# Performance work log

Measured on AMD Instinct MI355X. Metric: run time of the kernel, lower is better.

## Reference

```python
import jax, jax.numpy as jnp
import numpy as np

H = 1024   # hidden_dim
L = 2      # n_layers
V = 512    # dict_size['target']
B = 256    # batch
S = 512    # encoder seq len
IN = 64    # maxlen['input'][0] = encoder input feature dim
T = 64     # maxlen['target'] = decoder steps


def setup_inputs() -> dict:
    key = jax.random.key(0)
    ks = jax.random.split(key, 16)
    def p(k, shape):
        return jax.random.normal(k, shape, jnp.float32) * 0.05
    emb = p(ks[0], (V, H)).at[0].set(0.0)  # padding_idx=0 row is zero
    return dict(
        x=jax.random.normal(ks[1], (B, S, IN), jnp.float32),
        emb=emb,
        enc_Wih0=p(ks[2], (3 * H, IN)), enc_Whh0=p(ks[3], (3 * H, H)),
        enc_bih0=p(ks[4], (3 * H,)),   enc_bhh0=p(ks[5], (3 * H,)),
        enc_Wih1=p(ks[6], (3 * H, H)), enc_Whh1=p(ks[7], (3 * H, H)),
        enc_bih1=p(ks[8], (3 * H,)),   enc_bhh1=p(ks[9], (3 * H,)),
        dec_Wih=p(ks[10], (L, 3 * H, H)), dec_Whh=p(ks[11], (L, 3 * H, H)),
        dec_bih=p(ks[12], (L, 3 * H)),    dec_bhh=p(ks[13], (L, 3 * H)),
        fc_W=p(ks[14], (V, H)), fc_b=p(ks[15], (V,)),
    )


def gru_cell(x, h, Wih, Whh, bih, bhh):
    # torch GRU cell: r,z,n gate ordering
    gx = x @ Wih.T + bih            # (B, 3H)
    gh = h @ Whh.T + bhh            # (B, 3H)
    rx, zx, nx = jnp.split(gx, 3, axis=-1)
    rh, zh, nh = jnp.split(gh, 3, axis=-1)
    r = jax.nn.sigmoid(rx + rh)
    z = jax.nn.sigmoid(zx + zh)
    n = jnp.tanh(nx + r * nh)
    return (1.0 - z) * n + z * h


def reference(x, emb, enc_Wih0, enc_Whh0, enc_bih0, enc_bhh0,
              enc_Wih1, enc_Whh1, enc_bih1, enc_bhh1,
              dec_Wih, dec_Whh, dec_bih, dec_bhh, fc_W, fc_b):
    b = x.shape[0]
    # ---------- encoder: 2-layer unidirectional GRU ----------
    seq = jnp.swapaxes(x, 0, 1)  # (S, B, IN) time-major for scan
    enc_params = [(enc_Wih0, enc_Whh0, enc_bih0, enc_bhh0),
                  (enc_Wih1, enc_Whh1, enc_bih1, enc_bhh1)]
    finals = []
    for (Wih, Whh, bih, bhh) in enc_params:
        h0 = jnp.zeros((b, H), seq.dtype)
        def step(h, xt, Wih=Wih, Whh=Whh, bih=bih, bhh=bhh):
            hn = gru_cell(xt, h, Wih, Whh, bih, bhh)
            return hn, hn
        hT, seq = jax.lax.scan(step, h0, seq)
        finals.append(hT)
    hidden = jnp.stack(finals)  # (L, B, H)

    tok0 = jnp.zeros((b,), jnp.int32)  # start token 0 (== <pad>)

    def dec_step(carry, _):
        hcur, tok = carry
        inp = emb[tok]                       # (B, H) embedding lookup
        new_h = []
        for l in range(L):
            hn = gru_cell(inp, hcur[l], dec_Wih[l], dec_Whh[l],
                          dec_bih[l], dec_bhh[l])
            new_h.append(hn)
            inp = hn
        logits = inp @ fc_W.T + fc_b         # (B, V)
        tok = jnp.argmax(logits, axis=-1).astype(jnp.int32)
        return (jnp.stack(new_h), tok), logits

    (h_fin, _), logits_seq = jax.lax.scan(dec_step, (hidden, tok0), None, length=T)
    out = jnp.swapaxes(logits_seq, 0, 1)     # (B, T, V)
    return out, h_fin
```

## Files before the change

kernel.cpp:

```cpp
#include <hip/hip_runtime.h>
#include <math.h>

namespace {

constexpr int BSZ = 256;
constexpr int SEQ = 512;
constexpr int KIN = 64;
constexpr int HID = 1024;
constexpr int GD  = 3072;
constexpr int VOC = 512;
constexpr int TT  = 64;

typedef _Float16 half_t;
typedef _Float16 half8 __attribute__((ext_vector_type(8)));
typedef float f32x4 __attribute__((ext_vector_type(4)));

constexpr float LOSCL = 4096.f;
constexpr float LOINV = 1.f / 4096.f;

__device__ __forceinline__ void decode_mc(int bb, int& m0, int& c0) {
  int c_lo = bb & 7, rest = bb >> 3;
  int m = rest & 7, c_hi = rest >> 3;
  m0 = m * 32;
  c0 = (c_hi * 8 + c_lo) * 32;
}

__global__ __launch_bounds__(256) void swz_kernel(
    const float* __restrict__ src, half_t* __restrict__ hi,
    half_t* __restrict__ lo, int NG, int NKCH, int HIDR, int n)
{
  int i = blockIdx.x * 256 + threadIdx.x;
  if (i >= n) return;
  int j = i & 7, l = (i >> 3) & 63;
  int frag = i >> 9;
  int g = frag % NG;
  int rest = frag / NG;
  int w4 = rest & 3;
  int rest2 = rest >> 2;
  int kc = rest2 % NKCH;
  int ct = rest2 / NKCH;
  int ldw = NKCH * 64;
  int row = g * HIDR + ct * 32 + (w4 & 1) * 16 + (l & 15);
  int col = kc * 64 + (w4 >> 1) * 32 + (l >> 4) * 8 + j;
  float f = src[(size_t)row * ldw + col];
  half_t h = (half_t)f;
  hi[i] = h;
  lo[i] = (half_t)((f - (float)h) * LOSCL);
}

typedef half_t AldsT[2][2][32][136];

template<int NG, int G2>
__device__ __forceinline__ void gemm_swz128(
    const float* __restrict__ A, size_t lda, int nch,
    const half_t* __restrict__ Whi, const half_t* __restrict__ Wlo,
    int ct, int kc0, int nkch_tot, int m0,
    f32x4 (&aH)[4][2], f32x4 (&aL)[4][2], AldsT& Alds)
{
  const int tid = threadIdx.x;
  const int wv = tid >> 6, l = tid & 63, lr = l & 15, lk = l >> 4;
  const int colg = wv & 1, ksg = wv >> 1;
  const int arow = tid >> 3, aseg = tid & 7;
  const float* aptr = A + (size_t)(m0 + arow) * lda + aseg * 16;

  const size_t FR = (size_t)NG * 512;
  const size_t S2STR = 2 * FR;
  const size_t CSTR = 8 * FR;
  const size_t bbase =
      (((size_t)(ct * nkch_tot + kc0 + ksg)) * 4 + colg) * FR + l * 8;
  const half_t* bph = Whi + bbase;
  const half_t* bpl = Wlo + bbase;

  float4 paE[4], paO[4];
  half8 bhE[2 * NG], blE[2 * NG], bhO[2 * NG], blO[2 * NG];
  #pragma unroll
  for (int q = 0; q < 4; ++q) paE[q] = *(const float4*)(aptr + q * 4);
  #pragma unroll
  for (int s2 = 0; s2 < 2; ++s2)
    #pragma unroll
    for (int g = 0; g < NG; ++g) {
      bhE[s2 * NG + g] = *(const half8*)(bph + s2 * S2STR + g * 512);
      blE[s2 * NG + g] = *(const half8*)(bpl + s2 * S2STR + g * 512);
    }

#define SWC(pac, bhc, blc, pan, bhn, bln, CH, BUF)                            \
  {                                                                           \
    {               \
      float vals[16] = {pac[0].x, pac[0].y, pac[0].z, pac[0].w,               \
                        pac[1].x, pac[1].y, pac[1].z, pac[1].w,               \
                        pac[2].x, pac[2].y, pac[2].z, pac[2].w,               \
                        pac[3].x, pac[3].y, pac[3].z, pac[3].w};              \
      half8 hi8[2], lo8[2];                                                   \
      _Pragma("unroll") for (int j = 0; j < 16; ++j) {                        \
        float f = vals[j]; half_t h = (half_t)f;                              \
        hi8[j >> 3][j & 7] = h;                                               \
        lo8[j >> 3][j & 7] = (half_t)((f - (float)h) * LOSCL);                \
      }                                                                       \
      *(half8*)&Alds[BUF][0][arow][aseg * 16] = hi8[0];                       \
      *(half8*)&Alds[BUF][0][arow][aseg * 16 + 8] = hi8[1];                   \
      *(half8*)&Alds[BUF][1][arow][aseg * 16] = lo8[0];                       \
      *(half8*)&Alds[BUF][1][arow][aseg * 16 + 8] = lo8[1];                   \
    }                                                                         \
    __syncthreads();                                                          \
    if ((CH) + 1 < nch) {                                                     \
      _Pragma("unroll") for (int q = 0; q < 4; ++q)                           \
        pan[q] = *(const float4*)(aptr + ((CH) + 1) * 128 + q * 4);           \
      _Pragma("unroll") for (int s2 = 0; s2 < 2; ++s2)                        \
        _Pragma("unroll") for (int g = 0; g < NG; ++g) {                      \
          bhn[s2 * NG + g] =                                                  \
              *(const half8*)(bph + ((CH) + 1) * CSTR + s2 * S2STR + g * 512);\
          bln[s2 * NG + g] =                                                  \
              *(const half8*)(bpl + ((CH) + 1) * CSTR + s2 * S2STR + g * 512);\
        }                                                                     \
    }                                                                         \
    _Pragma("unroll") for (int s2 = 0; s2 < 2; ++s2) {                        \
      half8 ah0 = *(const half8*)&Alds[BUF][0][lr][ksg * 64 + s2 * 32 + lk * 8];      \
      half8 ah1 = *(const half8*)&Alds[BUF][0][16 + lr][ksg * 64 + s2 * 32 + lk * 8]; \
      half8 al0 = *(const half8*)&Alds[BUF][1][lr][ksg * 64 + s2 * 32 + lk * 8];      \
      half8 al1 = *(const half8*)&Alds[BUF][1][16 + lr][ksg * 64 + s2 * 32 + lk * 8]; \
      _Pragma("unroll") for (int g = 0; g < NG; ++g) {                        \
        const int slot = (g == 2) ? G2 : g;                                   \
        half8 bh = bhc[s2 * NG + g];                                          \
        half8 bl = blc[s2 * NG + g];                                          \
        aH[slot][0] = __builtin_amdgcn_mfma_f32_16x16x32_f16(ah0, bh, aH[slot][0], 0, 0, 0); \
        aH[slot][1] = __builtin_amdgcn_mfma_f32_16x16x32_f16(ah1, bh, aH[slot][1], 0, 0, 0); \
        aL[slot][0] = __builtin_amdgcn_mfma_f32_16x16x32_f16(ah0, bl, aL[slot][0], 0, 0, 0); \
        aL[slot][0] = __builtin_amdgcn_mfma_f32_16x16x32_f16(al0, bh, aL[slot][0], 0, 0, 0); \
        aL[slot][1] = __builtin_amdgcn_mfma_f32_16x16x32_f16(ah1, bl, aL[slot][1], 0, 0, 0); \
        aL[slot][1] = __builtin_amdgcn_mfma_f32_16x16x32_f16(al1, bh, aL[slot][1], 0, 0, 0); \
      }                                                                       \
    }                                                                         \
  }

  for (int ch = 0; ch < nch; ch += 2) {
    SWC(paE, bhE, blE, paO, bhO, blO, ch, 0)
    SWC(paO, bhO, blO, paE, bhE, blE, (ch + 1), 1)
  }
#undef SWC
}

template<int NG, int G2>
__device__ __forceinline__ void gemm_swz64(
    const float* __restrict__ A, size_t lda,
    const half_t* __restrict__ Whi, const half_t* __restrict__ Wlo,
    int ct, int nkch_tot, int m0,
    f32x4 (&aH)[4][2], f32x4 (&aL)[4][2], AldsT& Alds)
{
  const int tid = threadIdx.x;
  const int wv = tid >> 6, l = tid & 63, lr = l & 15, lk = l >> 4;
  const int colg = wv & 1, ksg = wv >> 1;
  const int arow = tid >> 3, aseg = tid & 7;
  const float* aptr = A + (size_t)(m0 + arow) * lda + aseg * 8;

  const size_t FR = (size_t)NG * 512;
  const size_t bbase =
      (((size_t)(ct * nkch_tot)) * 4 + (colg + 2 * ksg)) * FR + l * 8;
  half8 bh[NG], bl[NG];
  #pragma unroll
  for (int g = 0; g < NG; ++g) {
    bh[g] = *(const half8*)(Whi + bbase + g * 512);
    bl[g] = *(const half8*)(Wlo + bbase + g * 512);
  }
  float4 u0 = *(const float4*)(aptr);
  float4 u1 = *(const float4*)(aptr + 4);
  {
    float vals[8] = {u0.x, u0.y, u0.z, u0.w, u1.x, u1.y, u1.z, u1.w};
    half8 hi8, lo8;
    #pragma unroll
    for (int j = 0; j < 8; ++j) {
      float f = vals[j]; half_t h = (half_t)f;
      hi8[j] = h; lo8[j] = (half_t)((f - (float)h) * LOSCL);
    }
    *(half8*)&Alds[0][0][arow][aseg * 8] = hi8;
    *(half8*)&Alds[0][1][arow][aseg * 8] = lo8;
  }
  __syncthreads();
  half8 ah0 = *(const half8*)&Alds[0][0][lr][ksg * 32 + lk * 8];
  half8 ah1 = *(const half8*)&Alds[0][0][16 + lr][ksg * 32 + lk * 8];
  half8 al0 = *(const half8*)&Alds[0][1][lr][ksg * 32 + lk * 8];
  half8 al1 = *(const half8*)&Alds[0][1][16 + lr][ksg * 32 + lk * 8];
  #pragma unroll
  for (int g = 0; g < NG; ++g) {
    const int slot = (g == 2) ? G2 : g;
    aH[slot][0] = __builtin_amdgcn_mfma_f32_16x16x32_f16(ah0, bh[g], aH[slot][0], 0, 0, 0);
    aH[slot][1] = __builtin_amdgcn_mfma_f32_16x16x32_f16(ah1, bh[g], aH[slot][1], 0, 0, 0);
    aL[slot][0] = __builtin_amdgcn_mfma_f32_16x16x32_f16(ah0, bl[g], aL[slot][0], 0, 0, 0);
    aL[slot][0] = __builtin_amdgcn_mfma_f32_16x16x32_f16(al0, bh[g], aL[slot][0], 0, 0, 0);
    aL[slot][1] = __builtin_amdgcn_mfma_f32_16x16x32_f16(ah1, bl[g], aL[slot][1], 0, 0, 0);
    aL[slot][1] = __builtin_amdgcn_mfma_f32_16x16x32_f16(al1, bh[g], aL[slot][1], 0, 0, 0);
  }
}

template<int NS>
__device__ __forceinline__ void combine_ks(
    f32x4 (&aH)[4][2], f32x4 (&aL)[4][2], float* __restrict__ xch)
{
  const int tid = threadIdx.x;
  const int wv = tid >> 6, l = tid & 63;
  const int colg = wv & 1, ksg = wv >> 1;
  #pragma unroll
  for (int q = 0; q < NS; ++q)
    #pragma unroll
    for (int mf = 0; mf < 2; ++mf)
      aH[q][mf] = aH[q][mf] + aL[q][mf] * LOINV;
  __syncthreads();
  float* base = xch + ((size_t)colg * 64 + l) * (NS * 8);
  if (ksg == 1) {
    #pragma unroll
    for (int q = 0; q < NS; ++q)
      #pragma unroll
      for (int mf = 0; mf < 2; ++mf)
        *(f32x4*)(base + q * 8 + mf * 4) = aH[q][mf];
  }
  __syncthreads();
  if (ksg == 0) {
    #pragma unroll
    for (int q = 0; q < NS; ++q)
      #pragma unroll
      for (int mf = 0; mf < 2; ++mf)
        aH[q][mf] = aH[q][mf] + *(const f32x4*)(base + q * 8 + mf * 4);
  }
}

__device__ __forceinline__ void gru_epi32(
    f32x4 (&vv)[4][2],
    const float* __restrict__ bih, const float* __restrict__ bhh,
    const float* __restrict__ hprev, float* __restrict__ hout,
    int m0, int c0)
{
  const int tid = threadIdx.x;
  if (tid >= 128) return;
  const int wv = tid >> 6, l = tid & 63, lr = l & 15, lk = l >> 4;
  const int c = c0 + (wv & 1) * 16 + lr;
  float bhr = bhh[c], bhz = bhh[HID + c], bhn = bhh[2 * HID + c];
  float bir = 0.f, biz = 0.f, bin = 0.f;
  if (bih) { bir = bih[c]; biz = bih[HID + c]; bin = bih[2 * HID + c]; }
  #pragma unroll
  for (int mf = 0; mf < 2; ++mf) {
    #pragma unroll
    for (int i = 0; i < 4; ++i) {
      int b = m0 + mf * 16 + lk * 4 + i;
      float rs = vv[0][mf][i] + bhr + bir;
      float zs = vv[1][mf][i] + bhz + biz;
      float nx = vv[2][mf][i] + bin;
      float nh = vv[3][mf][i] + bhn;
      float r = 1.f / (1.f + expf(-rs));
      float z = 1.f / (1.f + expf(-zs));
      float n = tanhf(nx + r * nh);
      hout[(size_t)b * HID + c] =
          (1.f - z) * n + z * hprev[(size_t)b * HID + c];
    }
  }
}

__device__ __forceinline__ void write_partials32(
    f32x4 (&vv)[4][2], int s2, float* __restrict__ P, int m0, int c0)
{
  const int tid = threadIdx.x;
  if (tid >= 128) return;
  const int wv = tid >> 6, l = tid & 63, lr = l & 15, lk = l >> 4;
  const int c = c0 + (wv & 1) * 16 + lr;
  #pragma unroll
  for (int g = 0; g < 3; ++g) {
    const int slot = (g == 2) ? s2 : g;
    #pragma unroll
    for (int mf = 0; mf < 2; ++mf) {
      #pragma unroll
      for (int i = 0; i < 4; ++i) {
        int b = m0 + mf * 16 + lk * 4 + i;
        P[((size_t)g * BSZ + b) * HID + c] = vv[slot][mf][i];
      }
    }
  }
}

#define INIT_ACC(aH, aL)                                  \
  _Pragma("unroll") for (int q = 0; q < 4; ++q)           \
    _Pragma("unroll") for (int m_ = 0; m_ < 2; ++m_) {    \
      aH[q][m_] = (f32x4){0.f, 0.f, 0.f, 0.f};            \
      aL[q][m_] = (f32x4){0.f, 0.f, 0.f, 0.f};            \
    }

__global__ __launch_bounds__(256, 2) void enc_step_mfma(
    int s, const float* __restrict__ x,
    const half_t* __restrict__ Wih0h, const half_t* __restrict__ Wih0l,
    const float* __restrict__ bih0,
    const half_t* __restrict__ Whh0h, const half_t* __restrict__ Whh0l,
    const float* __restrict__ bhh0,
    const half_t* __restrict__ Wih1h, const half_t* __restrict__ Wih1l,
    const float* __restrict__ bih1,
    const half_t* __restrict__ Whh1h, const half_t* __restrict__ Whh1l,
    const float* __restrict__ bhh1,
    float* __restrict__ h0f, float* __restrict__ h1f)
{
  __shared__ __align__(16) AldsT Alds;
  f32x4 aH[4][2], aL[4][2];
  INIT_ACC(aH, aL)
  const size_t BH = (size_t)BSZ * HID;
  int blk = blockIdx.x;
  if (blk < 256) {
    if (s >= SEQ) return;
    int m0, c0; decode_mc(blk, m0, c0);
    int ct = c0 >> 5;
    const float* hp = h0f + ((s + 1) & 1) * BH;
    gemm_swz128<3, 3>(hp, HID, 8, Whh0h, Whh0l, ct, 0, 16, m0, aH, aL, Alds);
    gemm_swz64<3, 2>(x + (size_t)s * KIN, (size_t)SEQ * KIN, Wih0h, Wih0l,
                     ct, 1, m0, aH, aL, Alds);
    combine_ks<4>(aH, aL, (float*)Alds);
    gru_epi32(aH, bih0, bhh0, hp, h0f + (s & 1) * BH, m0, c0);
  } else {
    if (s < 1) return;
    int u = s - 1;
    int m0, c0; decode_mc(blk - 256, m0, c0);
    int ct = c0 >> 5;
    const float* hp = h1f + ((u + 1) & 1) * BH;
    const float* h0in = h0f + (u & 1) * BH;
    gemm_swz128<3, 3>(hp, HID, 8, Whh1h, Whh1l, ct, 0, 16, m0, aH, aL, Alds);
    gemm_swz128<3, 2>(h0in, HID, 8, Wih1h, Wih1l, ct, 0, 16, m0, aH, aL, Alds);
    combine_ks<4>(aH, aL, (float*)Alds);
    gru_epi32(aH, bih1, bhh1, hp, h1f + (u & 1) * BH, m0, c0);
  }
}

__global__ __launch_bounds__(256, 2) void gru0_main(
    const float* __restrict__ hprev,
    const half_t* __restrict__ Whhh, const half_t* __restrict__ Whhl,
    float* __restrict__ Pg)
{
  __shared__ __align__(16) AldsT Alds;
  f32x4 aH[4][2], aL[4][2];
  INIT_ACC(aH, aL)
  int bb = blockIdx.x;
  int kh = bb >> 8;
  int m0, c0; decode_mc(bb & 255, m0, c0);
  int ct = c0 >> 5;
  gemm_swz128<3, 3>(hprev + kh * 512, HID, 4, Whhh, Whhl, ct, kh * 8, 16, m0,
                    aH, aL, Alds);
  combine_ks<4>(aH, aL, (float*)Alds);
  write_partials32(aH, 3, Pg + (size_t)kh * 3 * BSZ * HID, m0, c0);
}

__global__ __launch_bounds__(256) void gru0_epi(
    const float* __restrict__ Pg, const float* __restrict__ bhh,
    const float* __restrict__ E, const int* __restrict__ tok,
    const float* __restrict__ hprev, float* __restrict__ hout)
{
  int idx = (blockIdx.x * 256 + threadIdx.x) * 4;
  int b = idx >> 10, c = idx & 1023;
  const size_t BH3 = (size_t)3 * BSZ * HID;
  float4 r0 = *(const float4*)&Pg[((size_t)0 * BSZ + b) * HID + c];
  float4 z0 = *(const float4*)&Pg[((size_t)1 * BSZ + b) * HID + c];
  float4 n0 = *(const float4*)&Pg[((size_t)2 * BSZ + b) * HID + c];
  float4 r1 = *(const float4*)&Pg[BH3 + ((size_t)0 * BSZ + b) * HID + c];
  float4 z1 = *(const float4*)&Pg[BH3 + ((size_t)1 * BSZ + b) * HID + c];
  float4 n1 = *(const float4*)&Pg[BH3 + ((size_t)2 * BSZ + b) * HID + c];
  const float* Er = E + (size_t)tok[b] * GD;
  float4 exr = *(const float4*)&Er[c];
  float4 exz = *(const float4*)&Er[HID + c];
  float4 exn = *(const float4*)&Er[2 * HID + c];
  float4 hp = *(const float4*)&hprev[(size_t)b * HID + c];
  float r0v[4] = {r0.x, r0.y, r0.z, r0.w}, z0v[4] = {z0.x, z0.y, z0.z, z0.w};
  float n0v[4] = {n0.x, n0.y, n0.z, n0.w}, r1v[4] = {r1.x, r1.y, r1.z, r1.w};
  float z1v[4] = {z1.x, z1.y, z1.z, z1.w}, n1v[4] = {n1.x, n1.y, n1.z, n1.w};
  float exrv[4] = {exr.x, exr.y, exr.z, exr.w};
  float exzv[4] = {exz.x, exz.y, exz.z, exz.w};
  float exnv[4] = {exn.x, exn.y, exn.z, exn.w};
  float hpv[4] = {hp.x, hp.y, hp.z, hp.w};
  float ov[4];
  #pragma unroll
  for (int j = 0; j < 4; ++j) {
    int cc = c + j;
    float rs = r0v[j] + r1v[j] + bhh[cc] + exrv[j];
    float zs = z0v[j] + z1v[j] + bhh[HID + cc] + exzv[j];
    float nh = n0v[j] + n1v[j] + bhh[2 * HID + cc];
    float r = 1.f / (1.f + expf(-rs));
    float z = 1.f / (1.f + expf(-zs));
    float n = tanhf(exnv[j] + r * nh);
    ov[j] = (1.f - z) * n + z * hpv[j];
  }
  float4 o; o.x = ov[0]; o.y = ov[1]; o.z = ov[2]; o.w = ov[3];
  *(float4*)&hout[(size_t)b * HID + c] = o;
}

__global__ __launch_bounds__(256, 2) void dec_l1_main(
    const float* __restrict__ hd1prev, const float* __restrict__ ho0,
    const half_t* __restrict__ Whhh, const half_t* __restrict__ Whhl,
    const half_t* __restrict__ Wihh, const half_t* __restrict__ Wihl,
    float* __restrict__ Phh, float* __restrict__ Pih)
{
  __shared__ __align__(16) AldsT Alds;
  f32x4 aH[4][2], aL[4][2];
  INIT_ACC(aH, aL)
  int bb = blockIdx.x;
  if (bb < 256) {
    int m0, c0; decode_mc(bb, m0, c0);
    gemm_swz128<3, 3>(hd1prev, HID, 8, Whhh, Whhl, c0 >> 5, 0, 16, m0,
                      aH, aL, Alds);
    combine_ks<4>(aH, aL, (float*)Alds);
    write_partials32(aH, 3, Phh, m0, c0);
  } else {
    int m0, c0; decode_mc(bb - 256, m0, c0);
    gemm_swz128<3, 2>(ho0, HID, 8, Wihh, Wihl, c0 >> 5, 0, 16, m0,
                      aH, aL, Alds);
    combine_ks<4>(aH, aL, (float*)Alds);
    write_partials32(aH, 2, Pih, m0, c0);
  }
}

__global__ __launch_bounds__(256) void dec_l1_epi(
    const float* __restrict__ Phh, const float* __restrict__ Pih,
    const float* __restrict__ bih, const float* __restrict__ bhh,
    const float* __restrict__ hprev, float* __restrict__ hout)
{
  int idx = (blockIdx.x * 256 + threadIdx.x) * 4;
  int b = idx >> 10, c = idx & 1023;
  float4 rh = *(const float4*)&Phh[((size_t)0 * BSZ + b) * HID + c];
  float4 zh = *(const float4*)&Phh[((size_t)1 * BSZ + b) * HID + c];
  float4 nh = *(const float4*)&Phh[((size_t)2 * BSZ + b) * HID + c];
  float4 rx = *(const float4*)&Pih[((size_t)0 * BSZ + b) * HID + c];
  float4 zx = *(const float4*)&Pih[((size_t)1 * BSZ + b) * HID + c];
  float4 nx = *(const float4*)&Pih[((size_t)2 * BSZ + b) * HID + c];
  float4 hp = *(const float4*)&hprev[(size_t)b * HID + c];
  float rhv[4] = {rh.x, rh.y, rh.z, rh.w}, zhv[4] = {zh.x, zh.y, zh.z, zh.w};
  float nhv[4] = {nh.x, nh.y, nh.z, nh.w}, rxv[4] = {rx.x, rx.y, rx.z, rx.w};
  float zxv[4] = {zx.x, zx.y, zx.z, zx.w}, nxv[4] = {nx.x, nx.y, nx.z, nx.w};
  float hpv[4] = {hp.x, hp.y, hp.z, hp.w};
  float ov[4];
  #pragma unroll
  for (int j = 0; j < 4; ++j) {
    int cc = c + j;
    float r = 1.f / (1.f + expf(-(rhv[j] + rxv[j] + bhh[cc] + bih[cc])));
    float z = 1.f / (1.f + expf(-(zhv[j] + zxv[j] + bhh[HID + cc] + bih[HID + cc])));
    float n = tanhf(nxv[j] + bih[2 * HID + cc] + r * (nhv[j] + bhh[2 * HID + cc]));
    ov[j] = (1.f - z) * n + z * hpv[j];
  }
  float4 o; o.x = ov[0]; o.y = ov[1]; o.z = ov[2]; o.w = ov[3];
  *(float4*)&hout[(size_t)b * HID + c] = o;
}

__global__ __launch_bounds__(256, 2) void fc_main(
    const float* __restrict__ h,
    const half_t* __restrict__ Wh, const half_t* __restrict__ Wl,
    float* __restrict__ Pfc)
{
  __shared__ __align__(16) AldsT Alds;
  f32x4 aH[4][2], aL[4][2];
  INIT_ACC(aH, aL)
  int bb = blockIdx.x;
  int kh = bb >> 7, sub = bb & 127;
  int v_lo = sub & 7, rest = sub >> 3;
  int m = rest & 7, v_hi = rest >> 3;
  int m0 = m * 32, v0 = (v_hi * 8 + v_lo) * 32;
  gemm_swz128<1, 0>(h + kh * 512, HID, 4, Wh, Wl, v0 >> 5, kh * 8, 16, m0,
                    aH, aL, Alds);
  combine_ks<1>(aH, aL, (float*)Alds);

  const int tid = threadIdx.x;
  if (tid >= 128) return;
  const int wv = tid >> 6, l = tid & 63, lr = l & 15, lk = l >> 4;
  int v = v0 + (wv & 1) * 16 + lr;
  float* P = Pfc + (size_t)kh * BSZ * VOC;
  #pragma unroll
  for (int mf = 0; mf < 2; ++mf) {
    #pragma unroll
    for (int i = 0; i < 4; ++i) {
      int b = m0 + mf * 16 + lk * 4 + i;
      P[(size_t)b * VOC + v] = aH[0][mf][i];
    }
  }
}

__global__ __launch_bounds__(256) void fc_epi(
    const float* __restrict__ Pfc, const float* __restrict__ fcb,
    float* __restrict__ out, int t, int* __restrict__ tok)
{
  __shared__ float sv[4];
  __shared__ int si[4];
  int b = blockIdx.x, tid = threadIdx.x;
  int va = tid, vb = tid + 256;
  float lga = Pfc[(size_t)b * VOC + va] + Pfc[((size_t)BSZ + b) * VOC + va] + fcb[va];
  float lgb = Pfc[(size_t)b * VOC + vb] + Pfc[((size_t)BSZ + b) * VOC + vb] + fcb[vb];
  out[((size_t)b * TT + t) * VOC + va] = lga;
  out[((size_t)b * TT + t) * VOC + vb] = lgb;
  float best = lga; int bi = va;
  if (lgb > best) { best = lgb; bi = vb; }
  #pragma unroll
  for (int off = 1; off < 64; off <<= 1) {
    float ov = __shfl_xor(best, off);
    int oi = __shfl_xor(bi, off);
    if (ov > best || (ov == best && oi < bi)) { best = ov; bi = oi; }
  }
  int wv = tid >> 6;
  if ((tid & 63) == 0) { sv[wv] = best; si[wv] = bi; }
  __syncthreads();
  if (tid == 0) {
    #pragma unroll
    for (int w = 1; w < 4; ++w)
      if (sv[w] > best || (sv[w] == best && si[w] < bi)) { best = sv[w]; bi = si[w]; }
    tok[b] = bi;
  }
}

__global__ __launch_bounds__(256) void e0_kernel(
    const float* __restrict__ emb, const float* __restrict__ Wih,
    const float* __restrict__ bih, float* __restrict__ E0)
{
  __shared__ float As[32][34];
  __shared__ float Bs[32][68];
  int m0 = (blockIdx.x & 15) << 5;
  int c0 = (blockIdx.x >> 4) << 6;
  int tid = threadIdx.x, tx = tid & 15, ty = tid >> 4;
  float acc[2][4] = {};
  for (int k0 = 0; k0 < HID; k0 += 32) {
    { int m = tid >> 3, kq = (tid & 7) << 2;
      float4 v = *(const float4*)(emb + (size_t)(m0 + m) * HID + k0 + kq);
      As[kq+0][m] = v.x; As[kq+1][m] = v.y; As[kq+2][m] = v.z; As[kq+3][m] = v.w; }
    #pragma unroll
    for (int r = 0; r < 2; ++r) {
      int idx = (r << 8) + tid;
      int n = idx >> 3, kq = (idx & 7) << 2;
      float4 v = *(const float4*)(Wih + (size_t)(c0 + n) * HID + k0 + kq);
      Bs[kq+0][n] = v.x; Bs[kq+1][n] = v.y; Bs[kq+2][n] = v.z; Bs[kq+3][n] = v.w;
    }
    __syncthreads();
    #pragma unroll 4
    for (int k = 0; k < 32; ++k) {
      float a0 = As[k][(ty << 1)], a1 = As[k][(ty << 1) + 1];
      float4 b = *(const float4*)&Bs[k][tx << 2];
      float bb[4] = {b.x, b.y, b.z, b.w};
      #pragma unroll
      for (int j = 0; j < 4; ++j) {
        acc[0][j] = fmaf(a0, bb[j], acc[0][j]);
        acc[1][j] = fmaf(a1, bb[j], acc[1][j]);
      }
    }
    __syncthreads();
  }
  #pragma unroll
  for (int i = 0; i < 2; ++i) {
    int v = m0 + (ty << 1) + i;
    #pragma unroll
    for (int j = 0; j < 4; ++j) {
      int g = c0 + (tx << 2) + j;
      E0[(size_t)v * GD + g] = acc[i][j] + bih[g];
    }
  }
}

}

extern "C" void kernel_launch(void* const* d_in, const int* in_sizes, int n_in,
                              void* d_out, int out_size, void* d_ws, size_t ws_size,
                              hipStream_t stream)
{
  const float* x     = (const float*)d_in[0];
  const float* emb   = (const float*)d_in[1];
  const float* eWih0 = (const float*)d_in[2];
  const float* eWhh0 = (const float*)d_in[3];
  const float* ebih0 = (const float*)d_in[4];
  const float* ebhh0 = (const float*)d_in[5];
  const float* eWih1 = (const float*)d_in[6];
  const float* eWhh1 = (const float*)d_in[7];
  const float* ebih1 = (const float*)d_in[8];
  const float* ebhh1 = (const float*)d_in[9];
  const float* dWih  = (const float*)d_in[10];
  const float* dWhh  = (const float*)d_in[11];
  const float* dbih  = (const float*)d_in[12];
  const float* dbhh  = (const float*)d_in[13];
  const float* fcW   = (const float*)d_in[14];
  const float* fcb   = (const float*)d_in[15];
  float* out = (float*)d_out;

  const size_t BH = (size_t)BSZ * HID;

  char* p = (char*)d_ws;
  auto alloc = [&](size_t bytes) {
    char* r = p; p += (bytes + 255) & ~(size_t)255; return r;
  };
  float* E0   = (float*)alloc((size_t)VOC * GD * 4);
  float* h0f  = (float*)alloc(2 * BH * 4);
  float* h1f  = (float*)alloc(2 * BH * 4);
  float* hd0f = (float*)alloc(2 * BH * 4);
  float* hd1f = (float*)alloc(2 * BH * 4);
  float* Phh  = (float*)alloc(3 * BH * 4);
  float* Pih  = (float*)alloc(3 * BH * 4);
  float* Pg   = (float*)alloc(6 * BH * 4);
  float* Pfc  = (float*)alloc((size_t)2 * BSZ * VOC * 4);
  const int NW_IH0 = GD * KIN, NW = GD * HID, NW_FC = VOC * HID;
  half_t* eWih0h = (half_t*)alloc((size_t)NW_IH0 * 2);
  half_t* eWih0l = (half_t*)alloc((size_t)NW_IH0 * 2);
  half_t* eWhh0h = (half_t*)alloc((size_t)NW * 2);
  half_t* eWhh0l = (half_t*)alloc((size_t)NW * 2);
  half_t* eWih1h = (half_t*)alloc((size_t)NW * 2);
  half_t* eWih1l = (half_t*)alloc((size_t)NW * 2);
  half_t* eWhh1h = (half_t*)alloc((size_t)NW * 2);
  half_t* eWhh1l = (half_t*)alloc((size_t)NW * 2);
  half_t* dWhh0h = (half_t*)alloc((size_t)NW * 2);
  half_t* dWhh0l = (half_t*)alloc((size_t)NW * 2);
  half_t* dWhh1h = (half_t*)alloc((size_t)NW * 2);
  half_t* dWhh1l = (half_t*)alloc((size_t)NW * 2);
  half_t* dWih1h = (half_t*)alloc((size_t)NW * 2);
  half_t* dWih1l = (half_t*)alloc((size_t)NW * 2);
  half_t* fcWh   = (half_t*)alloc((size_t)NW_FC * 2);
  half_t* fcWl   = (half_t*)alloc((size_t)NW_FC * 2);
  int* tok = (int*)alloc(BSZ * 4);

  hipMemsetAsync(h0f + BH, 0, BH * 4, stream);
  hipMemsetAsync(h1f + BH, 0, BH * 4, stream);
  hipMemsetAsync(tok, 0, BSZ * 4, stream);

  swz_kernel<<<NW_IH0 / 256, 256, 0, stream>>>(eWih0, eWih0h, eWih0l,
                                               3, 1, HID, NW_IH0);
  swz_kernel<<<NW / 256, 256, 0, stream>>>(eWhh0, eWhh0h, eWhh0l,
                                           3, 16, HID, NW);
  swz_kernel<<<NW / 256, 256, 0, stream>>>(eWih1, eWih1h, eWih1l,
                                           3, 16, HID, NW);
  swz_kernel<<<NW / 256, 256, 0, stream>>>(eWhh1, eWhh1h, eWhh1l,
                                           3, 16, HID, NW);
  swz_kernel<<<NW / 256, 256, 0, stream>>>(dWhh, dWhh0h, dWhh0l,
                                           3, 16, HID, NW);
  swz_kernel<<<NW / 256, 256, 0, stream>>>(dWhh + (size_t)NW, dWhh1h, dWhh1l,
                                           3, 16, HID, NW);
  swz_kernel<<<NW / 256, 256, 0, stream>>>(dWih + (size_t)NW, dWih1h, dWih1l,
                                           3, 16, HID, NW);
  swz_kernel<<<NW_FC / 256, 256, 0, stream>>>(fcW, fcWh, fcWl,
                                              1, 16, VOC, NW_FC);

  e0_kernel<<<768, 256, 0, stream>>>(emb, dWih, dbih, E0);

  for (int s = 0; s <= SEQ; ++s) {
    enc_step_mfma<<<512, 256, 0, stream>>>(
        s, x,
        eWih0h, eWih0l, ebih0, eWhh0h, eWhh0l, ebhh0,
        eWih1h, eWih1l, ebih1, eWhh1h, eWhh1l, ebhh1,
        h0f, h1f);
  }

  hipMemcpyAsync(hd0f + BH, h0f + BH, BH * 4, hipMemcpyDeviceToDevice, stream);
  hipMemcpyAsync(hd1f + BH, h1f + BH, BH * 4, hipMemcpyDeviceToDevice, stream);

  for (int t = 0; t < TT; ++t) {
    const float* hp0 = hd0f + ((t + 1) & 1) * BH;
    float* ho0 = hd0f + (t & 1) * BH;
    gru0_main<<<512, 256, 0, stream>>>(hp0, dWhh0h, dWhh0l, Pg);
    gru0_epi<<<256, 256, 0, stream>>>(Pg, dbhh, E0, tok, hp0, ho0);

    const float* hp1 = hd1f + ((t + 1) & 1) * BH;
    float* ho1 = hd1f + (t & 1) * BH;
    dec_l1_main<<<512, 256, 0, stream>>>(hp1, ho0, dWhh1h, dWhh1l,
                                         dWih1h, dWih1l, Phh, Pih);
    dec_l1_epi<<<256, 256, 0, stream>>>(Phh, Pih, dbih + GD, dbhh + GD,
                                        hp1, ho1);
    fc_main<<<256, 256, 0, stream>>>(ho1, fcWh, fcWl, Pfc);
    fc_epi<<<256, 256, 0, stream>>>(Pfc, fcb, out, t, tok);
  }

  hipMemcpyAsync(out + (size_t)BSZ * TT * VOC, hd0f + BH, BH * 4,
                 hipMemcpyDeviceToDevice, stream);
  hipMemcpyAsync(out + (size_t)BSZ * TT * VOC + BH, hd1f + BH, BH * 4,
                 hipMemcpyDeviceToDevice, stream);
}
```

Baseline: 17.14 ms.

## Double M-tile per block to 64 rows with 512-thread blocks sharing weight fragments

Blocks now cover 64 batch rows instead of 32, using 8 waves where the extra wave group handles the second 32-row half, so each weight column tile is read by half as many blocks. The A staging LDS buffer doubles, and grid sizes are halved while block size doubles for the encoder step, gru0_main and dec_l1_main. This is meant to cut redundant global loads of the hi/lo fp16 weight fragments. In exchange it uses more LDS per block, may reduce occupancy, and leaves fewer blocks to spread across CUs.

Result: slower. 20.28 ms (+18.3%).

```diff
diff --git a/kernel.cpp b/kernel.cpp
--- a/kernel.cpp
+++ b/kernel.cpp
@@ -18,10 +18,10 @@
 constexpr float LOSCL = 4096.f;
 constexpr float LOINV = 1.f / 4096.f;
 
-__device__ __forceinline__ void decode_mc(int bb, int& m0, int& c0) {
+__device__ __forceinline__ void decode_mc64(int bb, int& m0, int& c0) {
   int c_lo = bb & 7, rest = bb >> 3;
-  int m = rest & 7, c_hi = rest >> 3;
-  m0 = m * 32;
+  int m = rest & 3, c_hi = rest >> 2;
+  m0 = m * 64;
   c0 = (c_hi * 8 + c_lo) * 32;
 }
 
@@ -48,7 +48,7 @@
   lo[i] = (half_t)((f - (float)h) * LOSCL);
 }
 
-typedef half_t AldsT[2][2][32][136];
+typedef half_t AldsT[2][2][64][136];
 
 template<int NG, int G2>
 __device__ __forceinline__ void gemm_swz128(
@@ -59,7 +59,7 @@
 {
   const int tid = threadIdx.x;
   const int wv = tid >> 6, l = tid & 63, lr = l & 15, lk = l >> 4;
-  const int colg = wv & 1, ksg = wv >> 1;
+  const int colg = wv & 1, ksg = (wv >> 1) & 1, mg = wv >> 2;
   const int arow = tid >> 3, aseg = tid & 7;
   const float* aptr = A + (size_t)(m0 + arow) * lda + aseg * 16;
 
@@ -114,10 +114,10 @@
         }                                                                     \
     }                                                                         \
     _Pragma("unroll") for (int s2 = 0; s2 < 2; ++s2) {                        \
-      half8 ah0 = *(const half8*)&Alds[BUF][0][lr][ksg * 64 + s2 * 32 + lk * 8];      \
-      half8 ah1 = *(const half8*)&Alds[BUF][0][16 + lr][ksg * 64 + s2 * 32 + lk * 8]; \
-      half8 al0 = *(const half8*)&Alds[BUF][1][lr][ksg * 64 + s2 * 32 + lk * 8];      \
-      half8 al1 = *(const half8*)&Alds[BUF][1][16 + lr][ksg * 64 + s2 * 32 + lk * 8]; \
+      half8 ah0 = *(const half8*)&Alds[BUF][0][mg * 32 + lr][ksg * 64 + s2 * 32 + lk * 8];      \
+      half8 ah1 = *(const half8*)&Alds[BUF][0][mg * 32 + 16 + lr][ksg * 64 + s2 * 32 + lk * 8]; \
+      half8 al0 = *(const half8*)&Alds[BUF][1][mg * 32 + lr][ksg * 64 + s2 * 32 + lk * 8];      \
+      half8 al1 = *(const half8*)&Alds[BUF][1][mg * 32 + 16 + lr][ksg * 64 + s2 * 32 + lk * 8]; \
       _Pragma("unroll") for (int g = 0; g < NG; ++g) {                        \
         const int slot = (g == 2) ? G2 : g;                                   \
         half8 bh = bhc[s2 * NG + g];                                          \
@@ -148,7 +148,7 @@
 {
   const int tid = threadIdx.x;
   const int wv = tid >> 6, l = tid & 63, lr = l & 15, lk = l >> 4;
-  const int colg = wv & 1, ksg = wv >> 1;
+  const int colg = wv & 1, ksg = (wv >> 1) & 1, mg = wv >> 2;
   const int arow = tid >> 3, aseg = tid & 7;
   const float* aptr = A + (size_t)(m0 + arow) * lda + aseg * 8;
 
@@ -175,10 +175,10 @@
     *(half8*)&Alds[0][1][arow][aseg * 8] = lo8;
   }
   __syncthreads();
-  half8 ah0 = *(const half8*)&Alds[0][0][lr][ksg * 32 + lk * 8];
-  half8 ah1 = *(const half8*)&Alds[0][0][16 + lr][ksg * 32 + lk * 8];
-  half8 al0 = *(const half8*)&Alds[0][1][lr][ksg * 32 + lk * 8];
-  half8 al1 = *(const half8*)&Alds[0][1][16 + lr][ksg * 32 + lk * 8];
+  half8 ah0 = *(const half8*)&Alds[0][0][mg * 32 + lr][ksg * 32 + lk * 8];
+  half8 ah1 = *(const half8*)&Alds[0][0][mg * 32 + 16 + lr][ksg * 32 + lk * 8];
+  half8 al0 = *(const half8*)&Alds[0][1][mg * 32 + lr][ksg * 32 + lk * 8];
+  half8 al1 = *(const half8*)&Alds[0][1][mg * 32 + 16 + lr][ksg * 32 + lk * 8];
   #pragma unroll
   for (int g = 0; g < NG; ++g) {
     const int slot = (g == 2) ? G2 : g;
@@ -197,14 +197,14 @@
 {
   const int tid = threadIdx.x;
   const int wv = tid >> 6, l = tid & 63;
-  const int colg = wv & 1, ksg = wv >> 1;
+  const int colg = wv & 1, ksg = (wv >> 1) & 1, mg = wv >> 2;
   #pragma unroll
   for (int q = 0; q < NS; ++q)
     #pragma unroll
     for (int mf = 0; mf < 2; ++mf)
       aH[q][mf] = aH[q][mf] + aL[q][mf] * LOINV;
   __syncthreads();
-  float* base = xch + ((size_t)colg * 64 + l) * (NS * 8);
+  float* base = xch + ((size_t)(mg * 2 + colg) * 64 + l) * (NS * 8);
   if (ksg == 1) {
     #pragma unroll
     for (int q = 0; q < NS; ++q)
@@ -229,9 +229,10 @@
     int m0, int c0)
 {
   const int tid = threadIdx.x;
-  if (tid >= 128) return;
   const int wv = tid >> 6, l = tid & 63, lr = l & 15, lk = l >> 4;
-  const int c = c0 + (wv & 1) * 16 + lr;
+  const int colg = wv & 1, ksg = (wv >> 1) & 1, mg = wv >> 2;
+  if (ksg) return;
+  const int c = c0 + colg * 16 + lr;
   float bhr = bhh[c], bhz = bhh[HID + c], bhn = bhh[2 * HID + c];
   float bir = 0.f, biz = 0.f, bin = 0.f;
   if (bih) { bir = bih[c]; biz = bih[HID + c]; bin = bih[2 * HID + c]; }
@@ -239,7 +240,7 @@
   for (int mf = 0; mf < 2; ++mf) {
     #pragma unroll
     for (int i = 0; i < 4; ++i) {
-      int b = m0 + mf * 16 + lk * 4 + i;
+      int b = m0 + mg * 32 + mf * 16 + lk * 4 + i;
       float rs = vv[0][mf][i] + bhr + bir;
       float zs = vv[1][mf][i] + bhz + biz;
       float nx = vv[2][mf][i] + bin;
@@ -257,9 +258,10 @@
     f32x4 (&vv)[4][2], int s2, float* __restrict__ P, int m0, int c0)
 {
   const int tid = threadIdx.x;
-  if (tid >= 128) return;
   const int wv = tid >> 6, l = tid & 63, lr = l & 15, lk = l >> 4;
-  const int c = c0 + (wv & 1) * 16 + lr;
+  const int colg = wv & 1, ksg = (wv >> 1) & 1, mg = wv >> 2;
+  if (ksg) return;
+  const int c = c0 + colg * 16 + lr;
   #pragma unroll
   for (int g = 0; g < 3; ++g) {
     const int slot = (g == 2) ? s2 : g;
@@ -267,7 +269,7 @@
     for (int mf = 0; mf < 2; ++mf) {
       #pragma unroll
       for (int i = 0; i < 4; ++i) {
-        int b = m0 + mf * 16 + lk * 4 + i;
+        int b = m0 + mg * 32 + mf * 16 + lk * 4 + i;
         P[((size_t)g * BSZ + b) * HID + c] = vv[slot][mf][i];
       }
     }
@@ -281,7 +283,7 @@
       aL[q][m_] = (f32x4){0.f, 0.f, 0.f, 0.f};            \
     }
 
-__global__ __launch_bounds__(256, 2) void enc_step_mfma(
+__global__ __launch_bounds__(512, 2) void enc_step_mfma(
     int s, const float* __restrict__ x,
     const half_t* __restrict__ Wih0h, const half_t* __restrict__ Wih0l,
     const float* __restrict__ bih0,
@@ -298,9 +300,9 @@
   INIT_ACC(aH, aL)
   const size_t BH = (size_t)BSZ * HID;
   int blk = blockIdx.x;
-  if (blk < 256) {
+  if (blk < 128) {
     if (s >= SEQ) return;
-    int m0, c0; decode_mc(blk, m0, c0);
+    int m0, c0; decode_mc64(blk, m0, c0);
     int ct = c0 >> 5;
     const float* hp = h0f + ((s + 1) & 1) * BH;
     gemm_swz128<3, 3>(hp, HID, 8, Whh0h, Whh0l, ct, 0, 16, m0, aH, aL, Alds);
@@ -311,7 +313,7 @@
   } else {
     if (s < 1) return;
     int u = s - 1;
-    int m0, c0; decode_mc(blk - 256, m0, c0);
+    int m0, c0; decode_mc64(blk - 128, m0, c0);
     int ct = c0 >> 5;
     const float* hp = h1f + ((u + 1) & 1) * BH;
     const float* h0in = h0f + (u & 1) * BH;
@@ -322,7 +324,7 @@
   }
 }
 
-__global__ __launch_bounds__(256, 2) void gru0_main(
+__global__ __launch_bounds__(512, 2) void gru0_main(
     const float* __restrict__ hprev,
     const half_t* __restrict__ Whhh, const half_t* __restrict__ Whhl,
     float* __restrict__ Pg)
@@ -331,8 +333,8 @@
   f32x4 aH[4][2], aL[4][2];
   INIT_ACC(aH, aL)
   int bb = blockIdx.x;
-  int kh = bb >> 8;
-  int m0, c0; decode_mc(bb & 255, m0, c0);
+  int kh = bb >> 7;
+  int m0, c0; decode_mc64(bb & 127, m0, c0);
   int ct = c0 >> 5;
   gemm_swz128<3, 3>(hprev + kh * 512, HID, 4, Whhh, Whhl, ct, kh * 8, 16, m0,
                     aH, aL, Alds);
@@ -382,7 +384,7 @@
   *(float4*)&hout[(size_t)b * HID + c] = o;
 }
 
-__global__ __launch_bounds__(256, 2) void dec_l1_main(
+__global__ __launch_bounds__(512, 2) void dec_l1_main(
     const float* __restrict__ hd1prev, const float* __restrict__ ho0,
     const half_t* __restrict__ Whhh, const half_t* __restrict__ Whhl,
     const half_t* __restrict__ Wihh, const half_t* __restrict__ Wihl,
@@ -392,14 +394,14 @@
   f32x4 aH[4][2], aL[4][2];
   INIT_ACC(aH, aL)
   int bb = blockIdx.x;
-  if (bb < 256) {
-    int m0, c0; decode_mc(bb, m0, c0);
+  if (bb < 128) {
+    int m0, c0; decode_mc64(bb, m0, c0);
     gemm_swz128<3, 3>(hd1prev, HID, 8, Whhh, Whhl, c0 >> 5, 0, 16, m0,
                       aH, aL, Alds);
     combine_ks<4>(aH, aL, (float*)Alds);
     write_partials32(aH, 3, Phh, m0, c0);
   } else {
-    int m0, c0; decode_mc(bb - 256, m0, c0);
+    int m0, c0; decode_mc64(bb - 128, m0, c0);
     gemm_swz128<3, 2>(ho0, HID, 8, Wihh, Wihl, c0 >> 5, 0, 16, m0,
                       aH, aL, Alds);
     combine_ks<4>(aH, aL, (float*)Alds);
@@ -629,7 +631,7 @@
   e0_kernel<<<768, 256, 0, stream>>>(emb, dWih, dbih, E0);
 
   for (int s = 0; s <= SEQ; ++s) {
-    enc_step_mfma<<<512, 256, 0, stream>>>(
+    enc_step_mfma<<<256, 512, 0, stream>>>(
         s, x,
         eWih0h, eWih0l, ebih0, eWhh0h, eWhh0l, ebhh0,
         eWih1h, eWih1l, ebih1, eWhh1h, eWhh1l, ebhh1,
@@ -642,12 +644,12 @@
   for (int t = 0; t < TT; ++t) {
     const float* hp0 = hd0f + ((t + 1) & 1) * BH;
     float* ho0 = hd0f + (t & 1) * BH;
-    gru0_main<<<512, 256, 0, stream>>>(hp0, dWhh0h, dWhh0l, Pg);
+    gru0_main<<<256, 512, 0, stream>>>(hp0, dWhh0h, dWhh0l, Pg);
     gru0_epi<<<256, 256, 0, stream>>>(Pg, dbhh, E0, tok, hp0, ho0);
 
     const float* hp1 = hd1f + ((t + 1) & 1) * BH;
     float* ho1 = hd1f + (t & 1) * BH;
-    dec_l1_main<<<512, 256, 0, stream>>>(hp1, ho0, dWhh1h, dWhh1l,
+    dec_l1_main<<<256, 512, 0, stream>>>(hp1, ho0, dWhh1h, dWhh1l,
                                          dWih1h, dWih1l, Phh, Pih);
     dec_l1_epi<<<256, 256, 0, stream>>>(Phh, Pih, dbih + GD, dbhh + GD,
                                         hp1, ho1);
```
